# Kernel optimization log

Hardware: AMD Instinct MI355X
Metric: run time of the kernel (lower is better)

## Reference

```python
import jax, jax.numpy as jnp
import numpy as np

B, L, D, H = 4, 2048, 1024, 16
DH = D // H

def setup_inputs() -> dict:
    key = jax.random.key(0)
    k1, k2, k3 = jax.random.split(key, 3)
    x = jax.random.normal(k1, (B, L, D), dtype=jnp.float32)
    w_qkv = jax.random.normal(k2, (3 * D, D), dtype=jnp.float32) * (1.0 / np.sqrt(D))
    w_proj = jax.random.normal(k3, (D, D), dtype=jnp.float32) * (1.0 / np.sqrt(D))
    return {"x": x, "w_qkv": w_qkv, "w_proj": w_proj}

def reference(x, w_qkv, w_proj):
    b, l, d = x.shape
    scale = 1.0 / np.sqrt(DH)
    qkv = (x @ w_qkv.T).reshape(b, l, 3, H, DH)
    qkv = jnp.transpose(qkv, (2, 0, 3, 1, 4))
    q, k, v = qkv[0], qkv[1], qkv[2]
    scores = jnp.einsum('bhqd,bhkd->bhqk', q, k) * scale
    attn = jax.nn.softmax(scores, axis=-1)
    out = jnp.einsum('bhqk,bhkd->bhqd', attn, v)
    out = jnp.transpose(out, (0, 2, 1, 3)).reshape(b, l, d)
    return out @ w_proj.T
```

## Files before the change

### kernel.cpp

```cpp
#include <hip/hip_runtime.h>
#include <hip/hip_bf16.h>


typedef __bf16  bf16x8  __attribute__((ext_vector_type(8)));
typedef __bf16  bf16x4  __attribute__((ext_vector_type(4)));
typedef float   floatx4 __attribute__((ext_vector_type(4)));

__device__ __forceinline__ void async_ld16(const void* g, void* lds_base_uniform) {
  __builtin_amdgcn_global_load_lds(
      (const __attribute__((address_space(1))) void*)g,
      (__attribute__((address_space(3))) void*)lds_base_uniform,
      16, 0, 0);
}

__device__ __forceinline__ int detect_bf16(const void* p) {
  const unsigned short* u = (const unsigned short*)p;
  int sane = 0;
#pragma unroll 4
  for (int i = 0; i < 64; ++i) {
    unsigned short w = u[2 * i];
    int e = (w >> 7) & 0xFF;
    sane += (w == 0 || (e >= 100 && e <= 150)) ? 1 : 0;
  }
  return sane >= 32;
}

__device__ __forceinline__ bf16x8 ld8_f32cvt(const void* base, size_t elem) {
  const float* p = (const float*)base + elem;
  floatx4 u0 = *(const floatx4*)p;
  floatx4 u1 = *(const floatx4*)(p + 4);
  bf16x8 v;
  v[0] = (__bf16)u0[0]; v[1] = (__bf16)u0[1]; v[2] = (__bf16)u0[2]; v[3] = (__bf16)u0[3];
  v[4] = (__bf16)u1[0]; v[5] = (__bf16)u1[1]; v[6] = (__bf16)u1[2]; v[7] = (__bf16)u1[3];
  return v;
}

template<int CTRL>
__device__ __forceinline__ float dpp_f(float x) {
  return __builtin_bit_cast(float,
      __builtin_amdgcn_update_dpp(0, __builtin_bit_cast(int, x), CTRL, 0xF, 0xF, true));
}
__device__ __forceinline__ float row16_sum(float x) {
  x += dpp_f<0xB1>(x);
  x += dpp_f<0x4E>(x);
  x += dpp_f<0x141>(x);
  x += dpp_f<0x140>(x);
  return x;
}

__launch_bounds__(256)
__global__ void cvt3_kernel(const void* __restrict__ s0, __bf16* __restrict__ d0, int n0,
                            const void* __restrict__ s1, __bf16* __restrict__ d1, int n1,
                            const void* __restrict__ s2, __bf16* __restrict__ d2) {
  int u = blockIdx.x * blockDim.x + threadIdx.x;
  const void* src; __bf16* dst;
  if (u < n0)           { src = s0; dst = d0; }
  else if (u < n0 + n1) { src = s1; dst = d1; u -= n0; }
  else                  { src = s2; dst = d2; u -= n0 + n1; }
  const int is_bf16 = detect_bf16(src);
  const size_t e = (size_t)u * 8;
  if (is_bf16) *(bf16x8*)(dst + e) = *(const bf16x8*)((const __bf16*)src + e);
  else         *(bf16x8*)(dst + e) = ld8_f32cvt(src, e);
}

template<int EPI>
__launch_bounds__(256, 2)
__global__ void gemm_bt_kernel(const __bf16* __restrict__ A,
                               const __bf16* __restrict__ B,
                               const void* __restrict__ oprobe,
                               void* __restrict__ Cout,
                               __bf16* __restrict__ qb,
                               __bf16* __restrict__ kb,
                               __bf16* __restrict__ vtb,
                               int M, int N, int K)
{
  __shared__ __align__(16) __bf16 As[128 * 32];
  __shared__ __align__(16) __bf16 Bs[128 * 32];

  const int flat = blockIdx.x;
  const int m0 = (((flat & 7) << 3) | ((flat >> 3) & 7)) << 7;
  const int n0 = (flat >> 6) << 7;

  const int tid  = threadIdx.x;
  const int wave = tid >> 6;
  const int lane = tid & 63;
  const int quad = lane >> 4;
  const int l16  = lane & 15;
  const int wm   = wave >> 1;
  const int wn   = wave & 1;

  const int r_in   = lane >> 2;
  const int cchunk = lane & 3;

  const __bf16* Ab = A + (size_t)m0 * K;
  const __bf16* Bb = B + (size_t)n0 * K;

  floatx4 acc[4][4];
#pragma unroll
  for (int i = 0; i < 4; ++i)
#pragma unroll
    for (int j = 0; j < 4; ++j)
      acc[i][j] = (floatx4){0.f, 0.f, 0.f, 0.f};

  const int ca0 = wave * 2;
  for (int k0 = 0; k0 < K; k0 += 32) {
#pragma unroll
    for (int i = 0; i < 2; ++i) {
      const int ca  = ca0 + i;
      const int row = ca * 16 + r_in;
      async_ld16(Ab + (size_t)row * K + k0 + cchunk * 8, (char*)As + ca * 1024);
      async_ld16(Bb + (size_t)row * K + k0 + cchunk * 8, (char*)Bs + ca * 1024);
    }
    __syncthreads();

    bf16x8 af[4], bfr[4];
#pragma unroll
    for (int tt = 0; tt < 4; ++tt) {
      af[tt]  = *(const bf16x8*)&As[(wm * 64 + tt * 16 + l16) * 32 + quad * 8];
      bfr[tt] = *(const bf16x8*)&Bs[(wn * 64 + tt * 16 + l16) * 32 + quad * 8];
    }
#pragma unroll
    for (int mt = 0; mt < 4; ++mt)
#pragma unroll
      for (int nt = 0; nt < 4; ++nt)
        acc[mt][nt] = __builtin_amdgcn_mfma_f32_16x16x32_bf16(af[mt], bfr[nt], acc[mt][nt], 0, 0, 0);
    __syncthreads();
  }

  const int out_bf16 = (EPI == 1) ? detect_bf16(oprobe) : 0;

#pragma unroll
  for (int mt = 0; mt < 4; ++mt) {
#pragma unroll
    for (int nt = 0; nt < 4; ++nt) {
      const int n_idx = n0 + wn * 64 + nt * 16 + l16;
      const int mbase = m0 + wm * 64 + mt * 16 + quad * 4;
      if (EPI == 1) {
        if (out_bf16) {
#pragma unroll
          for (int r = 0; r < 4; ++r)
            ((__bf16*)Cout)[(size_t)(mbase + r) * N + n_idx] = (__bf16)acc[mt][nt][r];
        } else {
#pragma unroll
          for (int r = 0; r < 4; ++r)
            ((float*)Cout)[(size_t)(mbase + r) * N + n_idx] = acc[mt][nt][r];
        }
      } else {
        const int sel = n_idx >> 10;
        const int rem = n_idx & 1023;
        const int h   = rem >> 6;
        const int dh  = rem & 63;
        const int b   = mbase >> 11;
        const int l   = mbase & 2047;
        const int bh  = b * 16 + h;
        if (sel == 2) {
          bf16x4 pk;
#pragma unroll
          for (int r = 0; r < 4; ++r) pk[r] = (__bf16)acc[mt][nt][r];
          *(bf16x4*)&vtb[((size_t)bh * 64 + dh) * 2048 + l] = pk;
        } else {
          __bf16* dstb = (sel == 0 ? qb : kb) + ((size_t)bh * 2048 + l) * 64 + dh;
#pragma unroll
          for (int r = 0; r < 4; ++r)
            dstb[(size_t)r * 64] = (__bf16)acc[mt][nt][r];
        }
      }
    }
  }
}

__launch_bounds__(256, 4)
__global__ void attn_kernel(const __bf16* __restrict__ qb,
                            const __bf16* __restrict__ kb,
                            const __bf16* __restrict__ vtb,
                            __bf16* __restrict__ ob )
{
  __shared__ __align__(16) __bf16 S[2][2 * 64 * 72];

  const int tid  = threadIdx.x;
  const int wave = tid >> 6;
  const int lane = tid & 63;
  const int quad = lane >> 4;
  const int l16  = lane & 15;

  const int bh = blockIdx.y;
  const int q0 = blockIdx.x * 128;

  const __bf16* Qp = qb  + (size_t)bh * 2048 * 64;
  const __bf16* Kp = kb  + (size_t)bh * 2048 * 64;
  const __bf16* Vp = vtb + (size_t)bh * 64 * 2048;

  const float C1 = 0.125f * 1.44269504f;
  const float C2 = -8.0f  * 1.44269504f;

  bf16x8 aq[2][2];
#pragma unroll
  for (int rt = 0; rt < 2; ++rt) {
    const __bf16* qrow = Qp + (size_t)(q0 + wave * 32 + rt * 16 + l16) * 64;
    aq[rt][0] = *(const bf16x8*)(qrow + quad * 8);
    aq[rt][1] = *(const bf16x8*)(qrow + 32 + quad * 8);
  }

  bf16x8 onesb;
  {
    const __bf16 ov = (l16 == 0) ? (__bf16)1.0f : (__bf16)0.0f;
#pragma unroll
    for (int i = 0; i < 8; ++i) onesb[i] = ov;
  }

  floatx4 o[2][4], o5[2];
#pragma unroll
  for (int rt = 0; rt < 2; ++rt) {
    o5[rt] = (floatx4){0.f, 0.f, 0.f, 0.f};
#pragma unroll
    for (int dt = 0; dt < 4; ++dt) o[rt][dt] = (floatx4){0.f, 0.f, 0.f, 0.f};
  }

  const int sarr = wave >> 1;
  const int srb  = (wave & 1) * 32;
  const int sr0  = lane >> 3;
  const int scol = (lane & 7) * 8;

  {
    __bf16* dst = &S[0][sarr * (64 * 72)];
    if (sarr == 0) {
#pragma unroll
      for (int i = 0; i < 4; ++i) {
        const int row = srb + sr0 + 8 * i;
        *(bf16x8*)&dst[row * 72 + scol] = *(const bf16x8*)(Kp + (size_t)row * 64 + scol);
      }
    } else {
#pragma unroll
      for (int i = 0; i < 4; ++i) {
        const int row = srb + sr0 + 8 * i;
        *(bf16x8*)&dst[row * 72 + scol] = *(const bf16x8*)(Vp + (size_t)row * 2048 + scol);
      }
    }
  }
  __syncthreads();

  for (int kt = 0; kt < 32; ++kt) {
    const int cur = kt & 1;
    const int nxt = cur ^ 1;
    const int kn  = (((kt + 1) & 31) << 6);

    bf16x8 sreg[4];
    if (sarr == 0) {
#pragma unroll
      for (int i = 0; i < 4; ++i) {
        const int row = srb + sr0 + 8 * i;
        sreg[i] = *(const bf16x8*)(Kp + (size_t)(kn + row) * 64 + scol);
      }
    } else {
#pragma unroll
      for (int i = 0; i < 4; ++i) {
        const int row = srb + sr0 + 8 * i;
        sreg[i] = *(const bf16x8*)(Vp + (size_t)row * 2048 + kn + scol);
      }
    }

    const __bf16* Kc = &S[cur][0];
    const __bf16* Vc = &S[cur][64 * 72];
    __bf16*       Pq = &S[nxt][0] + wave * 2304;

    floatx4 st[2][4];
    __builtin_amdgcn_s_setprio(1);
#pragma unroll
    for (int nt = 0; nt < 4; ++nt) {
      const int krow = nt * 16 + l16;
      bf16x8 ak0 = *(const bf16x8*)&Kc[krow * 72 + quad * 8];
      bf16x8 ak1 = *(const bf16x8*)&Kc[krow * 72 + 32 + quad * 8];
#pragma unroll
      for (int rt = 0; rt < 2; ++rt) {
        floatx4 z = (floatx4){0.f, 0.f, 0.f, 0.f};
        z = __builtin_amdgcn_mfma_f32_16x16x32_bf16(ak0, aq[rt][0], z, 0, 0, 0);
        z = __builtin_amdgcn_mfma_f32_16x16x32_bf16(ak1, aq[rt][1], z, 0, 0, 0);
        st[rt][nt] = z;
      }
    }
    __builtin_amdgcn_s_setprio(0);

#pragma unroll
    for (int rt = 0; rt < 2; ++rt) {
#pragma unroll
      for (int nt = 0; nt < 4; ++nt) {
        bf16x4 pk;
#pragma unroll
        for (int r = 0; r < 4; ++r)
          pk[r] = (__bf16)__builtin_amdgcn_exp2f(fmaf(st[rt][nt][r], C1, C2));
        *(bf16x4*)&Pq[(rt * 16 + l16) * 72 + nt * 16 + quad * 4] = pk;
      }
    }

    __builtin_amdgcn_wave_barrier();

    bf16x8 ap[2][2];
#pragma unroll
    for (int rt = 0; rt < 2; ++rt) {
      ap[rt][0] = *(const bf16x8*)&Pq[(rt * 16 + l16) * 72 + quad * 8];
      ap[rt][1] = *(const bf16x8*)&Pq[(rt * 16 + l16) * 72 + 32 + quad * 8];
    }

    __builtin_amdgcn_s_setprio(1);
#pragma unroll
    for (int dt = 0; dt < 4; ++dt) {
      const int vrow = dt * 16 + l16;
      bf16x8 bv0 = *(const bf16x8*)&Vc[vrow * 72 + quad * 8];
      bf16x8 bv1 = *(const bf16x8*)&Vc[vrow * 72 + 32 + quad * 8];
#pragma unroll
      for (int rt = 0; rt < 2; ++rt) {
        o[rt][dt] = __builtin_amdgcn_mfma_f32_16x16x32_bf16(ap[rt][0], bv0, o[rt][dt], 0, 0, 0);
        o[rt][dt] = __builtin_amdgcn_mfma_f32_16x16x32_bf16(ap[rt][1], bv1, o[rt][dt], 0, 0, 0);
      }
    }
#pragma unroll
    for (int rt = 0; rt < 2; ++rt) {
      o5[rt] = __builtin_amdgcn_mfma_f32_16x16x32_bf16(ap[rt][0], onesb, o5[rt], 0, 0, 0);
      o5[rt] = __builtin_amdgcn_mfma_f32_16x16x32_bf16(ap[rt][1], onesb, o5[rt], 0, 0, 0);
    }
    __builtin_amdgcn_s_setprio(0);

    __builtin_amdgcn_wave_barrier();

    {
      __bf16* dst = &S[nxt][sarr * (64 * 72)];
#pragma unroll
      for (int i = 0; i < 4; ++i) {
        const int row = srb + sr0 + 8 * i;
        *(bf16x8*)&dst[row * 72 + scol] = sreg[i];
      }
    }
    __syncthreads();
  }

  const int b = bh >> 4;
  const int h = bh & 15;
#pragma unroll
  for (int rt = 0; rt < 2; ++rt)
#pragma unroll
    for (int r = 0; r < 4; ++r) {
      const float lv  = row16_sum(l16 == 0 ? o5[rt][r] : 0.f);
      const float inv = 1.f / lv;
      const size_t rowbase =
          ((size_t)b * 2048 + q0 + wave * 32 + rt * 16 + quad * 4 + r) * 1024 + h * 64;
#pragma unroll
      for (int dt = 0; dt < 4; ++dt)
        ob[rowbase + dt * 16 + l16] = (__bf16)(o[rt][dt][r] * inv);
    }
}

extern "C" void kernel_launch(void* const* d_in, const int* in_sizes, int n_in,
                              void* d_out, int out_size, void* d_ws, size_t ws_size,
                              hipStream_t stream)
{
  (void)in_sizes; (void)n_in; (void)out_size; (void)ws_size;

  const void* x     = d_in[0];
  const void* wqkv  = d_in[1];
  const void* wproj = d_in[2];

  const size_t NX    = (size_t)8192 * 1024;
  const size_t NWQKV = (size_t)3072 * 1024;
  const size_t NWPRJ = (size_t)1024 * 1024;

  __bf16* qbuf   = (__bf16*)d_ws;
  __bf16* kbuf   = qbuf + NX;
  __bf16* vtbuf  = kbuf + NX;
  __bf16* abuf   = vtbuf + NX;
  __bf16* xb     = abuf + NX;
  __bf16* wqkvb  = xb + NX;
  __bf16* wprojb = wqkvb + NWQKV;

  dim3 blk(256);

  cvt3_kernel<<<dim3((NX + NWQKV + NWPRJ) / 2048), blk, 0, stream>>>(
      x, xb, NX / 8, wqkv, wqkvb, NWQKV / 8, wproj, wprojb);

  gemm_bt_kernel<0><<<dim3(24 * 64), blk, 0, stream>>>(
      xb, wqkvb, nullptr, nullptr, qbuf, kbuf, vtbuf, 8192, 3072, 1024);

  attn_kernel<<<dim3(2048 / 128, 64), blk, 0, stream>>>(qbuf, kbuf, vtbuf, abuf);

  gemm_bt_kernel<1><<<dim3(8 * 64), blk, 0, stream>>>(
      abuf, wprojb, wproj, d_out, nullptr, nullptr, nullptr, 8192, 1024, 1024);
}
```

Measured before the change: 283.2 us.

## Store Q/K as row-major token layout via LDS-staged epilogue; single-lane dtype detect

The QKV GEMM epilogue now stages Q and K tiles through LDS and writes them as 16-byte vector stores into a combined [B*L, 2048] row-major buffer. This replaces scattered 2-byte stores into per-head [BH, L, 64] arrays. The attention kernel reads Q/K with a 2048-element row stride, so each row of its loads is now a separate 128-byte segment instead of contiguous memory. The cvt kernel also runs the bf16 detection probe on one lane per wave and broadcasts it with readfirstlane, cutting redundant probe loads.

```diff
diff --git a/kernel.cpp b/kernel.cpp
--- a/kernel.cpp
+++ b/kernel.cpp
@@ -57,7 +57,9 @@
   if (u < n0)           { src = s0; dst = d0; }
   else if (u < n0 + n1) { src = s1; dst = d1; u -= n0; }
   else                  { src = s2; dst = d2; u -= n0 + n1; }
-  const int is_bf16 = detect_bf16(src);
+  const int lane = threadIdx.x & 63;
+  int det = (lane == 0) ? detect_bf16(src) : 0;
+  const int is_bf16 = __builtin_amdgcn_readfirstlane(det);
   const size_t e = (size_t)u * 8;
   if (is_bf16) *(bf16x8*)(dst + e) = *(const bf16x8*)((const __bf16*)src + e);
   else         *(bf16x8*)(dst + e) = ld8_f32cvt(src, e);
@@ -69,13 +71,13 @@
                                const __bf16* __restrict__ B,
                                const void* __restrict__ oprobe,
                                void* __restrict__ Cout,
-                               __bf16* __restrict__ qb,
-                               __bf16* __restrict__ kb,
+                               __bf16* __restrict__ qkb,
                                __bf16* __restrict__ vtb,
                                int M, int N, int K)
 {
-  __shared__ __align__(16) __bf16 As[128 * 32];
-  __shared__ __align__(16) __bf16 Bs[128 * 32];
+  __shared__ __align__(16) __bf16 SM[9216];
+  __bf16* As = SM;
+  __bf16* Bs = SM + 4096;
 
   const int flat = blockIdx.x;
   const int m0 = (((flat & 7) << 3) | ((flat >> 3) & 7)) << 7;
@@ -127,15 +129,14 @@
     __syncthreads();
   }
 
-  const int out_bf16 = (EPI == 1) ? detect_bf16(oprobe) : 0;
-
-#pragma unroll
-  for (int mt = 0; mt < 4; ++mt) {
-#pragma unroll
-    for (int nt = 0; nt < 4; ++nt) {
-      const int n_idx = n0 + wn * 64 + nt * 16 + l16;
-      const int mbase = m0 + wm * 64 + mt * 16 + quad * 4;
-      if (EPI == 1) {
+  if (EPI == 1) {
+    const int out_bf16 = detect_bf16(oprobe);
+#pragma unroll
+    for (int mt = 0; mt < 4; ++mt) {
+#pragma unroll
+      for (int nt = 0; nt < 4; ++nt) {
+        const int n_idx = n0 + wn * 64 + nt * 16 + l16;
+        const int mbase = m0 + wm * 64 + mt * 16 + quad * 4;
         if (out_bf16) {
 #pragma unroll
           for (int r = 0; r < 4; ++r)
@@ -145,24 +146,50 @@
           for (int r = 0; r < 4; ++r)
             ((float*)Cout)[(size_t)(mbase + r) * N + n_idx] = acc[mt][nt][r];
         }
-      } else {
-        const int sel = n_idx >> 10;
-        const int rem = n_idx & 1023;
-        const int h   = rem >> 6;
-        const int dh  = rem & 63;
-        const int b   = mbase >> 11;
-        const int l   = mbase & 2047;
-        const int bh  = b * 16 + h;
-        if (sel == 2) {
+      }
+    }
+  } else {
+    const int sel = n0 >> 10;
+    if (sel < 2) {
+      __bf16* eQ = SM + wave * (16 * 72);
+      const int ncol = n0 + wn * 64;
+      const int mb   = m0 + wm * 64;
+      const int rl   = lane >> 3;
+      const int ch   = lane & 7;
+#pragma unroll
+      for (int mt = 0; mt < 4; ++mt) {
+#pragma unroll
+        for (int nt = 0; nt < 4; ++nt)
+#pragma unroll
+          for (int r = 0; r < 4; ++r)
+            eQ[(quad * 4 + r) * 72 + nt * 16 + l16] = (__bf16)acc[mt][nt][r];
+        __builtin_amdgcn_wave_barrier();
+#pragma unroll
+        for (int i = 0; i < 2; ++i) {
+          const int row = rl + 8 * i;
+          bf16x8 v = *(const bf16x8*)&eQ[row * 72 + ch * 8];
+          const size_t m = (size_t)(mb + mt * 16 + row);
+          *(bf16x8*)&qkb[m * 2048 + ncol + ch * 8] = v;
+        }
+        __builtin_amdgcn_wave_barrier();
+      }
+    } else {
+#pragma unroll
+      for (int mt = 0; mt < 4; ++mt) {
+#pragma unroll
+        for (int nt = 0; nt < 4; ++nt) {
+          const int n_idx = n0 + wn * 64 + nt * 16 + l16;
+          const int mbase = m0 + wm * 64 + mt * 16 + quad * 4;
+          const int rem = n_idx & 1023;
+          const int h   = rem >> 6;
+          const int dh  = rem & 63;
+          const int b   = mbase >> 11;
+          const int l   = mbase & 2047;
+          const int bh  = b * 16 + h;
           bf16x4 pk;
 #pragma unroll
           for (int r = 0; r < 4; ++r) pk[r] = (__bf16)acc[mt][nt][r];
           *(bf16x4*)&vtb[((size_t)bh * 64 + dh) * 2048 + l] = pk;
-        } else {
-          __bf16* dstb = (sel == 0 ? qb : kb) + ((size_t)bh * 2048 + l) * 64 + dh;
-#pragma unroll
-          for (int r = 0; r < 4; ++r)
-            dstb[(size_t)r * 64] = (__bf16)acc[mt][nt][r];
         }
       }
     }
@@ -170,8 +197,7 @@
 }
 
 __launch_bounds__(256, 4)
-__global__ void attn_kernel(const __bf16* __restrict__ qb,
-                            const __bf16* __restrict__ kb,
+__global__ void attn_kernel(const __bf16* __restrict__ qkb,
                             const __bf16* __restrict__ vtb,
                             __bf16* __restrict__ ob )
 {
@@ -184,10 +210,12 @@
   const int l16  = lane & 15;
 
   const int bh = blockIdx.y;
+  const int b  = bh >> 4;
+  const int h  = bh & 15;
   const int q0 = blockIdx.x * 128;
 
-  const __bf16* Qp = qb  + (size_t)bh * 2048 * 64;
-  const __bf16* Kp = kb  + (size_t)bh * 2048 * 64;
+  const __bf16* Qp = qkb + (size_t)b * 2048 * 2048 + h * 64;
+  const __bf16* Kp = Qp + 1024;
   const __bf16* Vp = vtb + (size_t)bh * 64 * 2048;
 
   const float C1 = 0.125f * 1.44269504f;
@@ -196,7 +224,7 @@
   bf16x8 aq[2][2];
 #pragma unroll
   for (int rt = 0; rt < 2; ++rt) {
-    const __bf16* qrow = Qp + (size_t)(q0 + wave * 32 + rt * 16 + l16) * 64;
+    const __bf16* qrow = Qp + (size_t)(q0 + wave * 32 + rt * 16 + l16) * 2048;
     aq[rt][0] = *(const bf16x8*)(qrow + quad * 8);
     aq[rt][1] = *(const bf16x8*)(qrow + 32 + quad * 8);
   }
@@ -227,7 +255,7 @@
 #pragma unroll
       for (int i = 0; i < 4; ++i) {
         const int row = srb + sr0 + 8 * i;
-        *(bf16x8*)&dst[row * 72 + scol] = *(const bf16x8*)(Kp + (size_t)row * 64 + scol);
+        *(bf16x8*)&dst[row * 72 + scol] = *(const bf16x8*)(Kp + (size_t)row * 2048 + scol);
       }
     } else {
 #pragma unroll
@@ -249,7 +277,7 @@
 #pragma unroll
       for (int i = 0; i < 4; ++i) {
         const int row = srb + sr0 + 8 * i;
-        sreg[i] = *(const bf16x8*)(Kp + (size_t)(kn + row) * 64 + scol);
+        sreg[i] = *(const bf16x8*)(Kp + (size_t)(kn + row) * 2048 + scol);
       }
     } else {
 #pragma unroll
@@ -333,8 +361,6 @@
     __syncthreads();
   }
 
-  const int b = bh >> 4;
-  const int h = bh & 15;
 #pragma unroll
   for (int rt = 0; rt < 2; ++rt)
 #pragma unroll
@@ -363,9 +389,8 @@
   const size_t NWQKV = (size_t)3072 * 1024;
   const size_t NWPRJ = (size_t)1024 * 1024;
 
-  __bf16* qbuf   = (__bf16*)d_ws;
-  __bf16* kbuf   = qbuf + NX;
-  __bf16* vtbuf  = kbuf + NX;
+  __bf16* qkbuf  = (__bf16*)d_ws;
+  __bf16* vtbuf  = qkbuf + 2 * NX;
   __bf16* abuf   = vtbuf + NX;
   __bf16* xb     = abuf + NX;
   __bf16* wqkvb  = xb + NX;
@@ -377,10 +402,10 @@
       x, xb, NX / 8, wqkv, wqkvb, NWQKV / 8, wproj, wprojb);
 
   gemm_bt_kernel<0><<<dim3(24 * 64), blk, 0, stream>>>(
-      xb, wqkvb, nullptr, nullptr, qbuf, kbuf, vtbuf, 8192, 3072, 1024);
-
-  attn_kernel<<<dim3(2048 / 128, 64), blk, 0, stream>>>(qbuf, kbuf, vtbuf, abuf);
+      xb, wqkvb, nullptr, nullptr, qkbuf, vtbuf, 8192, 3072, 1024);
+
+  attn_kernel<<<dim3(2048 / 128, 64), blk, 0, stream>>>(qkbuf, vtbuf, abuf);
 
   gemm_bt_kernel<1><<<dim3(8 * 64), blk, 0, stream>>>(
-      abuf, wprojb, wproj, d_out, nullptr, nullptr, nullptr, 8192, 1024, 1024);
-}
+      abuf, wprojb, wproj, d_out, nullptr, nullptr, 8192, 1024, 1024);
+}
```

Result: no change. 285.3 us (+0.7%).

## Load V operands directly from global into registers and swizzle attention block order

Applied to the files above, without the earlier changes.

The attention kernel no longer stages V^T tiles through LDS. Each wave now loads its MFMA B-operand fragments for V straight from global memory into registers every iteration, while K alone is double-buffered in LDS and the P scratch gets its own dedicated LDS region. The grid is flattened to 1D with a swizzle so that blocks launched together fall on different heads, which is meant to spread L2 and channel load. This cuts LDS traffic and shared-memory size but makes each wave issue redundant V global loads and exposes their latency within the iteration.

```diff
diff --git a/kernel.cpp b/kernel.cpp
--- a/kernel.cpp
+++ b/kernel.cpp
@@ -175,7 +175,8 @@
                             const __bf16* __restrict__ vtb,
                             __bf16* __restrict__ ob )
 {
-  __shared__ __align__(16) __bf16 S[2][2 * 64 * 72];
+  __shared__ __align__(16) __bf16 Ks[2][64 * 72];
+  __shared__ __align__(16) __bf16 Ps[4][32 * 72];
 
   const int tid  = threadIdx.x;
   const int wave = tid >> 6;
@@ -183,8 +184,12 @@
   const int quad = lane >> 4;
   const int l16  = lane & 15;
 
-  const int bh = blockIdx.y;
-  const int q0 = blockIdx.x * 128;
+  const int flat = blockIdx.x;
+  const int swz  = (flat & 7) * 128 + (flat >> 3);
+  const int bh   = swz >> 4;
+  const int q0   = (swz & 15) * 128;
+  const int b    = bh >> 4;
+  const int h    = bh & 15;
 
   const __bf16* Qp = qb  + (size_t)bh * 2048 * 64;
   const __bf16* Kp = kb  + (size_t)bh * 2048 * 64;
@@ -216,26 +221,13 @@
     for (int dt = 0; dt < 4; ++dt) o[rt][dt] = (floatx4){0.f, 0.f, 0.f, 0.f};
   }
 
-  const int sarr = wave >> 1;
-  const int srb  = (wave & 1) * 32;
-  const int sr0  = lane >> 3;
-  const int scol = (lane & 7) * 8;
-
-  {
-    __bf16* dst = &S[0][sarr * (64 * 72)];
-    if (sarr == 0) {
-#pragma unroll
-      for (int i = 0; i < 4; ++i) {
-        const int row = srb + sr0 + 8 * i;
-        *(bf16x8*)&dst[row * 72 + scol] = *(const bf16x8*)(Kp + (size_t)row * 64 + scol);
-      }
-    } else {
-#pragma unroll
-      for (int i = 0; i < 4; ++i) {
-        const int row = srb + sr0 + 8 * i;
-        *(bf16x8*)&dst[row * 72 + scol] = *(const bf16x8*)(Vp + (size_t)row * 2048 + scol);
-      }
-    }
+  const int sr0  = tid >> 3;
+  const int scol = (tid & 7) * 8;
+
+#pragma unroll
+  for (int i = 0; i < 2; ++i) {
+    const int row = sr0 + 32 * i;
+    *(bf16x8*)&Ks[0][row * 72 + scol] = *(const bf16x8*)(Kp + (size_t)row * 64 + scol);
   }
   __syncthreads();
 
@@ -244,24 +236,23 @@
     const int nxt = cur ^ 1;
     const int kn  = (((kt + 1) & 31) << 6);
 
-    bf16x8 sreg[4];
-    if (sarr == 0) {
-#pragma unroll
-      for (int i = 0; i < 4; ++i) {
-        const int row = srb + sr0 + 8 * i;
-        sreg[i] = *(const bf16x8*)(Kp + (size_t)(kn + row) * 64 + scol);
-      }
-    } else {
-#pragma unroll
-      for (int i = 0; i < 4; ++i) {
-        const int row = srb + sr0 + 8 * i;
-        sreg[i] = *(const bf16x8*)(Vp + (size_t)row * 2048 + kn + scol);
-      }
-    }
-
-    const __bf16* Kc = &S[cur][0];
-    const __bf16* Vc = &S[cur][64 * 72];
-    __bf16*       Pq = &S[nxt][0] + wave * 2304;
+    bf16x8 kreg[2];
+#pragma unroll
+    for (int i = 0; i < 2; ++i) {
+      const int row = sr0 + 32 * i;
+      kreg[i] = *(const bf16x8*)(Kp + (size_t)(kn + row) * 64 + scol);
+    }
+
+    bf16x8 vb[4][2];
+#pragma unroll
+    for (int dt = 0; dt < 4; ++dt) {
+      const __bf16* vr = Vp + (size_t)(dt * 16 + l16) * 2048 + (kt << 6);
+      vb[dt][0] = *(const bf16x8*)(vr + quad * 8);
+      vb[dt][1] = *(const bf16x8*)(vr + 32 + quad * 8);
+    }
+
+    const __bf16* Kc = &Ks[cur][0];
+    __bf16*       Pq = &Ps[wave][0];
 
     floatx4 st[2][4];
     __builtin_amdgcn_s_setprio(1);
@@ -304,13 +295,10 @@
     __builtin_amdgcn_s_setprio(1);
 #pragma unroll
     for (int dt = 0; dt < 4; ++dt) {
-      const int vrow = dt * 16 + l16;
-      bf16x8 bv0 = *(const bf16x8*)&Vc[vrow * 72 + quad * 8];
-      bf16x8 bv1 = *(const bf16x8*)&Vc[vrow * 72 + 32 + quad * 8];
 #pragma unroll
       for (int rt = 0; rt < 2; ++rt) {
-        o[rt][dt] = __builtin_amdgcn_mfma_f32_16x16x32_bf16(ap[rt][0], bv0, o[rt][dt], 0, 0, 0);
-        o[rt][dt] = __builtin_amdgcn_mfma_f32_16x16x32_bf16(ap[rt][1], bv1, o[rt][dt], 0, 0, 0);
+        o[rt][dt] = __builtin_amdgcn_mfma_f32_16x16x32_bf16(ap[rt][0], vb[dt][0], o[rt][dt], 0, 0, 0);
+        o[rt][dt] = __builtin_amdgcn_mfma_f32_16x16x32_bf16(ap[rt][1], vb[dt][1], o[rt][dt], 0, 0, 0);
       }
     }
 #pragma unroll
@@ -320,21 +308,14 @@
     }
     __builtin_amdgcn_s_setprio(0);
 
-    __builtin_amdgcn_wave_barrier();
-
-    {
-      __bf16* dst = &S[nxt][sarr * (64 * 72)];
-#pragma unroll
-      for (int i = 0; i < 4; ++i) {
-        const int row = srb + sr0 + 8 * i;
-        *(bf16x8*)&dst[row * 72 + scol] = sreg[i];
-      }
+#pragma unroll
+    for (int i = 0; i < 2; ++i) {
+      const int row = sr0 + 32 * i;
+      *(bf16x8*)&Ks[nxt][row * 72 + scol] = kreg[i];
     }
     __syncthreads();
   }
 
-  const int b = bh >> 4;
-  const int h = bh & 15;
 #pragma unroll
   for (int rt = 0; rt < 2; ++rt)
 #pragma unroll
@@ -379,7 +360,7 @@
   gemm_bt_kernel<0><<<dim3(24 * 64), blk, 0, stream>>>(
       xb, wqkvb, nullptr, nullptr, qbuf, kbuf, vtbuf, 8192, 3072, 1024);
 
-  attn_kernel<<<dim3(2048 / 128, 64), blk, 0, stream>>>(qbuf, kbuf, vtbuf, abuf);
+  attn_kernel<<<dim3(1024), blk, 0, stream>>>(qbuf, kbuf, vtbuf, abuf);
 
   gemm_bt_kernel<1><<<dim3(8 * 64), blk, 0, stream>>>(
       abuf, wprojb, wproj, d_out, nullptr, nullptr, nullptr, 8192, 1024, 1024);
```

New measurement: 491.9 us. +73.7%, slower.
